# Performance work log

Measured on AMD Instinct MI355X. Metric: run time of the kernel, lower is better.

The kernel has to match this reference:

```python
import jax, jax.numpy as jnp
import numpy as np

N_SRC = 50000
N_DST = 50000
E = 800000
D = 128
OUT = 128


def setup_inputs() -> dict:
    key = jax.random.key(0)
    k1, k2, k3, k4, k5, k6 = jax.random.split(key, 6)
    lim = 1.0 / np.sqrt(D)
    return {
        "x_src": jax.random.normal(k1, (N_SRC, D), dtype=jnp.float32),
        "x_dst": jax.random.normal(k2, (N_DST, D), dtype=jnp.float32),
        "edge_src": jax.random.randint(k3, (E,), 0, N_SRC, dtype=jnp.int64),
        "edge_dst": jax.random.randint(k4, (E,), 0, N_DST, dtype=jnp.int64),
        "num_dst": N_DST,
        # learned params (torch nn.Linear: y = x @ W.T + b), stored here as [in, out]
        "W_neigh": jax.random.uniform(k5, (D, OUT), jnp.float32, -lim, lim),
        "b_neigh": jnp.zeros((OUT,), jnp.float32),
        "W_self": jax.random.uniform(k6, (D, OUT), jnp.float32, -lim, lim),
        "b_self": jnp.zeros((OUT,), jnp.float32),
    }


def reference(x_src, x_dst, edge_src, edge_dst, num_dst, W_neigh, b_neigh, W_self, b_self):
    # gather source features per edge: [E, D]
    neigh_feats = x_src[edge_src]
    # scatter-mean onto destination nodes
    summed = jax.ops.segment_sum(neigh_feats, edge_dst, num_segments=num_dst)  # [num_dst, D]
    count = jax.ops.segment_sum(jnp.ones((edge_dst.shape[0], 1), x_src.dtype), edge_dst,
                                num_segments=num_dst)
    agg = summed / jnp.clip(count, 1.0)
    # dual linear + add
    return agg @ W_neigh + b_neigh + x_dst @ W_self + b_self
```

## Files before the change

### kernel.cpp

```cpp
#include <hip/hip_runtime.h>

#define D 128
#define TM 64
#define RPT 2
#define CBITS 7
#define CSIZE 128
#define MAXNB 512
#define CAPB 2560
#define EPB 2048

typedef __attribute__((ext_vector_type(8))) short bf16x8;
typedef __attribute__((ext_vector_type(4))) float f32x4;


__device__ __forceinline__ unsigned short f32_to_bf16(float x) {
    unsigned u = __float_as_uint(x);
    u += 0x7FFFu + ((u >> 16) & 1u);
    return (unsigned short)(u >> 16);
}
__device__ __forceinline__ float bf16_to_f32(unsigned short h) {
    return __uint_as_float(((unsigned)h) << 16);
}

__global__ __launch_bounds__(256) void prep_kernel(
    const float* __restrict__ Wn, const float* __restrict__ Ws,
    unsigned short* __restrict__ Wtn, unsigned short* __restrict__ Wts,
    int* __restrict__ gcursor, int NB) {
    const int stride = gridDim.x * 256;
    for (int i = blockIdx.x * 256 + threadIdx.x; i < D * D; i += stride) {
        int n = i >> 7, k = i & (D - 1);
        Wtn[i] = f32_to_bf16(Wn[k * D + n]);
        Wts[i] = f32_to_bf16(Ws[k * D + n]);
    }
    for (int i = blockIdx.x * 256 + threadIdx.x; i < NB; i += stride)
        gcursor[i] = 0;
}

__global__ __launch_bounds__(256) void fused_part_gemm_kernel(
    const int* __restrict__ edge_src, const int* __restrict__ edge_dst,
    int* __restrict__ gcursor, int* __restrict__ packed, int E, int NB,
    const float* __restrict__ x_src, const float* __restrict__ x_dst,
    const unsigned short* __restrict__ Wtn, const unsigned short* __restrict__ Wts,
    const float* __restrict__ bn, const float* __restrict__ bs,
    unsigned short* __restrict__ y16, float* __restrict__ out,
    int M_SRC, int N, int nblk, int blkA, int pstride) {
    __shared__ __align__(16) char smem[TM * 136 * 2 + D * 136 * 2];
    const int t = threadIdx.x;
    const int idx = (int)blockIdx.x;

    const bool isPart = (idx % pstride == 0) && (idx / pstride < nblk);

    if (isPart) {
        const int pid = idx / pstride;
        int* lh    = (int*)smem;
        int* lbase = lh + MAXNB;
        for (int i = t; i < NB; i += 256) lh[i] = 0;
        __syncthreads();
        const int base = pid * EPB;
        int es[8], ed[8], rk[8];
        #pragma unroll
        for (int i = 0; i < 8; ++i) {
            int e = base + t + i * 256;
            if (e < E) { es[i] = edge_src[e]; ed[i] = edge_dst[e]; }
            else ed[i] = -1;
        }
        #pragma unroll
        for (int i = 0; i < 8; ++i)
            if (ed[i] >= 0) rk[i] = atomicAdd(&lh[ed[i] >> CBITS], 1);
        __syncthreads();
        for (int i = t; i < NB; i += 256) {
            int v = lh[i];
            lbase[i] = v ? atomicAdd(&gcursor[i], v) : 0;
        }
        __syncthreads();
        #pragma unroll
        for (int i = 0; i < 8; ++i) {
            if (ed[i] >= 0) {
                int bk = ed[i] >> CBITS;
                int pos = lbase[bk] + rk[i];
                if (pos < CAPB)
                    packed[(size_t)bk * CAPB + pos] =
                        (es[i] << CBITS) | (ed[i] & (CSIZE - 1));
            }
        }
        return;
    }

    typedef unsigned short ushort136[136];
    ushort136* LA = (ushort136*)smem;
    ushort136* LW = (ushort136*)(smem + TM * 136 * 2);

    const int npb  = min((idx + pstride - 1) / pstride, nblk);
    const int gb   = idx - npb;
    const bool isA  = gb < blkA;
    const int  base0 = (isA ? gb : gb - blkA) * (TM * RPT);
    const int  M    = isA ? M_SRC : N;
    const float* Ap = isA ? x_src : x_dst;
    const unsigned short* Wp = isA ? Wtn : Wts;

    {
        const int4* Wv = (const int4*)Wp;
        #pragma unroll
        for (int i = 0; i < 8; ++i) {
            int vi = t + i * 256;
            int r = vi >> 4, c8 = vi & 15;
            *(int4*)&LW[r][c8 * 8] = Wv[vi];
        }
    }

    const int lane = t & 63;
    const int wv   = t >> 6;
    const int wr   = wv & 1;
    const int wc   = wv >> 1;
    const int lr   = lane & 15;
    const int g    = lane >> 4;

    #pragma unroll
    for (int half = 0; half < RPT; ++half) {
        const int row0 = base0 + half * TM;
        {
            const float4* Av = (const float4*)Ap;
            #pragma unroll
            for (int i = 0; i < 8; ++i) {
                int vi = t + i * 256;
                int r = vi >> 5, c4 = vi & 31;
                int sr = min(row0 + r, M - 1);
                float4 v = Av[(size_t)sr * 32 + c4];
                ushort4 p;
                p.x = f32_to_bf16(v.x); p.y = f32_to_bf16(v.y);
                p.z = f32_to_bf16(v.z); p.w = f32_to_bf16(v.w);
                *(ushort4*)&LA[r][c4 * 4] = p;
            }
        }
        __syncthreads();

        f32x4 acc[2][4];
        #pragma unroll
        for (int i = 0; i < 2; ++i)
            #pragma unroll
            for (int j = 0; j < 4; ++j) acc[i][j] = (f32x4){0.f, 0.f, 0.f, 0.f};

        #pragma unroll
        for (int kt = 0; kt < 4; ++kt) {
            bf16x8 b0 = *(const bf16x8*)&LW[wc * 64 + 0 * 16 + lr][kt * 32 + g * 8];
            bf16x8 b1 = *(const bf16x8*)&LW[wc * 64 + 1 * 16 + lr][kt * 32 + g * 8];
            bf16x8 b2 = *(const bf16x8*)&LW[wc * 64 + 2 * 16 + lr][kt * 32 + g * 8];
            bf16x8 b3 = *(const bf16x8*)&LW[wc * 64 + 3 * 16 + lr][kt * 32 + g * 8];
            bf16x8 a0 = *(const bf16x8*)&LA[wr * 32 + lr][kt * 32 + g * 8];
            bf16x8 a1 = *(const bf16x8*)&LA[wr * 32 + 16 + lr][kt * 32 + g * 8];
            acc[0][0] = __builtin_amdgcn_mfma_f32_16x16x32_bf16(a0, b0, acc[0][0], 0, 0, 0);
            acc[0][1] = __builtin_amdgcn_mfma_f32_16x16x32_bf16(a0, b1, acc[0][1], 0, 0, 0);
            acc[0][2] = __builtin_amdgcn_mfma_f32_16x16x32_bf16(a0, b2, acc[0][2], 0, 0, 0);
            acc[0][3] = __builtin_amdgcn_mfma_f32_16x16x32_bf16(a0, b3, acc[0][3], 0, 0, 0);
            acc[1][0] = __builtin_amdgcn_mfma_f32_16x16x32_bf16(a1, b0, acc[1][0], 0, 0, 0);
            acc[1][1] = __builtin_amdgcn_mfma_f32_16x16x32_bf16(a1, b1, acc[1][1], 0, 0, 0);
            acc[1][2] = __builtin_amdgcn_mfma_f32_16x16x32_bf16(a1, b2, acc[1][2], 0, 0, 0);
            acc[1][3] = __builtin_amdgcn_mfma_f32_16x16x32_bf16(a1, b3, acc[1][3], 0, 0, 0);
        }

        if (isA) {
            #pragma unroll
            for (int i = 0; i < 2; ++i) {
                #pragma unroll
                for (int j = 0; j < 4; ++j) {
                    int col = wc * 64 + j * 16 + lr;
                    #pragma unroll
                    for (int r = 0; r < 4; ++r) {
                        int row = row0 + wr * 32 + i * 16 + g * 4 + r;
                        if (row < M)
                            y16[(size_t)row * D + col] = f32_to_bf16(acc[i][j][r]);
                    }
                }
            }
        } else {
            #pragma unroll
            for (int i = 0; i < 2; ++i) {
                #pragma unroll
                for (int j = 0; j < 4; ++j) {
                    int col = wc * 64 + j * 16 + lr;
                    float bias = bn[col] + bs[col];
                    #pragma unroll
                    for (int r = 0; r < 4; ++r) {
                        int row = row0 + wr * 32 + i * 16 + g * 4 + r;
                        if (row < M)
                            out[(size_t)row * D + col] = acc[i][j][r] + bias;
                    }
                }
            }
        }
        if (half + 1 < RPT) __syncthreads();
    }
}

__global__ __launch_bounds__(512) void fine_kernel(
    const int* __restrict__ packed, const int* __restrict__ gcursor,
    int* __restrict__ off_beg, int* __restrict__ off_end,
    int* __restrict__ eidx, int N) {
    __shared__ int dcount[8][CSIZE];
    __shared__ int wbase[8][CSIZE];
    __shared__ int sbuf[CSIZE];
    const int b  = blockIdx.x;
    const int d0 = b << CBITS;
    const int beg = b * CAPB;
    const int cnt = min(gcursor[b], CAPB);
    const int t = threadIdx.x;
    const int wv = t >> 6;

    if (t < CSIZE) {
        #pragma unroll
        for (int w = 0; w < 8; ++w) dcount[w][t] = 0;
    }
    __syncthreads();
    for (int i = t; i < cnt; i += 512)
        atomicAdd(&dcount[wv][packed[beg + i] & (CSIZE - 1)], 1);
    __syncthreads();
    int tot = 0;
    if (t < CSIZE) {
        #pragma unroll
        for (int w = 0; w < 8; ++w) tot += dcount[w][t];
        sbuf[t] = tot;
    }
    __syncthreads();
    for (int ofs = 1; ofs < CSIZE; ofs <<= 1) {
        int u = (t < CSIZE && t >= ofs) ? sbuf[t - ofs] : 0;
        __syncthreads();
        if (t < CSIZE) sbuf[t] += u;
        __syncthreads();
    }
    if (t < CSIZE) {
        int excl = sbuf[t] - tot;
        int d = d0 + t;
        if (d < N) {
            off_beg[d] = beg + excl;
            off_end[d] = beg + excl + tot;
        }
        int run = excl;
        #pragma unroll
        for (int w = 0; w < 8; ++w) {
            wbase[w][t] = run;
            run += dcount[w][t];
        }
    }
    __syncthreads();
    for (int i = t; i < cnt; i += 512) {
        int p = packed[beg + i];
        int pos = beg + atomicAdd(&wbase[wv][p & (CSIZE - 1)], 1);
        eidx[pos] = p >> CBITS;
    }
}

__global__ __launch_bounds__(256) void gather_out_kernel(
    const unsigned short* __restrict__ y16,
    const int* __restrict__ off_beg,
    const int* __restrict__ off_end,
    const int* __restrict__ eidx,
    float* __restrict__ out, int N) {
    const int wave = (int)(((long long)blockIdx.x * blockDim.x + threadIdx.x) >> 6);
    const int lane = threadIdx.x & 63;
    if (wave >= N) return;
    const int h = lane >> 4;
    const int c = lane & 15;
    const int beg = off_beg[wave];
    const int end = off_end[wave];

    float acc[8];
    #pragma unroll
    for (int j = 0; j < 8; ++j) acc[j] = 0.f;

    int i = beg + h;
    for (; i + 4 < end; i += 8) {
        int s0 = eidx[i];
        int s1 = eidx[i + 4];
        const int4 v0 = *reinterpret_cast<const int4*>(y16 + (size_t)s0 * D + c * 8);
        const int4 v1 = *reinterpret_cast<const int4*>(y16 + (size_t)s1 * D + c * 8);
        const unsigned short* h0 = (const unsigned short*)&v0;
        const unsigned short* h1 = (const unsigned short*)&v1;
        #pragma unroll
        for (int j = 0; j < 8; ++j)
            acc[j] += bf16_to_f32(h0[j]) + bf16_to_f32(h1[j]);
    }
    if (i < end) {
        int s = eidx[i];
        const int4 v = *reinterpret_cast<const int4*>(y16 + (size_t)s * D + c * 8);
        const unsigned short* hs = (const unsigned short*)&v;
        #pragma unroll
        for (int j = 0; j < 8; ++j) acc[j] += bf16_to_f32(hs[j]);
    }

    #pragma unroll
    for (int j = 0; j < 8; ++j) {
        acc[j] += __shfl_down(acc[j], 32);
        acc[j] += __shfl_down(acc[j], 16);
    }

    if (h == 0) {
        const float inv = 1.0f / fmaxf((float)(end - beg), 1.0f);
        float4* o = reinterpret_cast<float4*>(out + (size_t)wave * D) + c * 2;
        float4 c0 = o[0], c1 = o[1];
        c0.x = fmaf(acc[0], inv, c0.x);
        c0.y = fmaf(acc[1], inv, c0.y);
        c0.z = fmaf(acc[2], inv, c0.z);
        c0.w = fmaf(acc[3], inv, c0.w);
        c1.x = fmaf(acc[4], inv, c1.x);
        c1.y = fmaf(acc[5], inv, c1.y);
        c1.z = fmaf(acc[6], inv, c1.z);
        c1.w = fmaf(acc[7], inv, c1.w);
        o[0] = c0;
        o[1] = c1;
    }
}

extern "C" void kernel_launch(void* const* d_in, const int* in_sizes, int n_in,
                              void* d_out, int out_size, void* d_ws, size_t ws_size,
                              hipStream_t stream) {
    const float* x_src    = (const float*)d_in[0];
    const float* x_dst    = (const float*)d_in[1];
    const int*   edge_src = (const int*)d_in[2];
    const int*   edge_dst = (const int*)d_in[3];
    const float* Wn = (const float*)d_in[5];
    const float* bn = (const float*)d_in[6];
    const float* Ws = (const float*)d_in[7];
    const float* bs = (const float*)d_in[8];

    const int E     = in_sizes[2];
    const int N     = in_sizes[1] / D;
    const int M_SRC = in_sizes[0] / D;

    const int NB   = (N + CSIZE - 1) >> CBITS;
    const int nblk = (E + EPB - 1) / EPB;

    unsigned short* y16 = (unsigned short*)d_ws;
    unsigned short* Wtn = y16 + (size_t)M_SRC * D;
    unsigned short* Wts = Wtn + D * D;
    int* packed  = (int*)(Wts + D * D);
    int* eidx    = packed + (size_t)NB * CAPB;
    int* off_beg = eidx + (size_t)NB * CAPB;
    int* off_end = off_beg + N;
    int* gcursor = off_end + N;

    const int T = 256;
    prep_kernel<<<32, T, 0, stream>>>(Wn, Ws, Wtn, Wts, gcursor, NB);

    const int ROWS = TM * RPT;
    const int blkA = (M_SRC + ROWS - 1) / ROWS;
    const int blkB = (N + ROWS - 1) / ROWS;
    const int total = nblk + blkA + blkB;
    const int pstride = total / nblk > 1 ? total / nblk : 1;
    fused_part_gemm_kernel<<<total, T, 0, stream>>>(
        edge_src, edge_dst, gcursor, packed, E, NB,
        x_src, x_dst, Wtn, Wts, bn, bs, y16, (float*)d_out,
        M_SRC, N, nblk, blkA, pstride);

    fine_kernel<<<NB, 512, 0, stream>>>(packed, gcursor, off_beg, off_end, eidx, N);

    gather_out_kernel<<<(N + 3) / 4, T, 0, stream>>>(
        y16, off_beg, off_end, eidx, (float*)d_out, N);
}
```

Before: 73.77 us.

## Quantize projected source rows to int8 with per-row scales for gather

The projected source features are now stored as int8 with a per-row fp32 scale instead of bf16. Each row's scale comes from a cross-wave absmax reduction staged through shared memory, and rows are written out with coalesced 16-byte stores. The gather kernel reads 16 int8 values per lane plus a scale, which roughly halves the random-gather traffic per edge. The cost is extra syncs and reductions in the GEMM epilogue, plus lower accuracy from int8 quantization that could exceed tolerance.

```diff
diff --git a/kernel.cpp b/kernel.cpp
--- a/kernel.cpp
+++ b/kernel.cpp
@@ -42,7 +42,7 @@
     const float* __restrict__ x_src, const float* __restrict__ x_dst,
     const unsigned short* __restrict__ Wtn, const unsigned short* __restrict__ Wts,
     const float* __restrict__ bn, const float* __restrict__ bs,
-    unsigned short* __restrict__ y16, float* __restrict__ out,
+    char* __restrict__ y8, float* __restrict__ scale_g, float* __restrict__ out,
     int M_SRC, int N, int nblk, int blkA, int pstride) {
     __shared__ __align__(16) char smem[TM * 136 * 2 + D * 136 * 2];
     const int t = threadIdx.x;
@@ -159,18 +159,62 @@
         }
 
         if (isA) {
+            float pmax[2][4];
+            #pragma unroll
+            for (int i = 0; i < 2; ++i)
+                #pragma unroll
+                for (int r = 0; r < 4; ++r) {
+                    float m = fabsf(acc[i][0][r]);
+                    m = fmaxf(m, fabsf(acc[i][1][r]));
+                    m = fmaxf(m, fabsf(acc[i][2][r]));
+                    m = fmaxf(m, fabsf(acc[i][3][r]));
+                    pmax[i][r] = m;
+                }
+            #pragma unroll
+            for (int mask = 1; mask <= 8; mask <<= 1)
+                #pragma unroll
+                for (int i = 0; i < 2; ++i)
+                    #pragma unroll
+                    for (int r = 0; r < 4; ++r)
+                        pmax[i][r] = fmaxf(pmax[i][r], __shfl_xor(pmax[i][r], mask));
+            __syncthreads();
+            float* rmax = (float*)(smem + 8192);
+            char*  st8  = smem;
+            if (lr == 0) {
+                #pragma unroll
+                for (int i = 0; i < 2; ++i)
+                    #pragma unroll
+                    for (int r = 0; r < 4; ++r)
+                        rmax[wc * 64 + wr * 32 + i * 16 + g * 4 + r] = pmax[i][r];
+            }
+            __syncthreads();
             #pragma unroll
             for (int i = 0; i < 2; ++i) {
                 #pragma unroll
-                for (int j = 0; j < 4; ++j) {
-                    int col = wc * 64 + j * 16 + lr;
+                for (int r = 0; r < 4; ++r) {
+                    int rl = wr * 32 + i * 16 + g * 4 + r;
+                    float mx = fmaxf(rmax[rl], rmax[64 + rl]);
+                    float inv = mx > 0.f ? 127.f / mx : 0.f;
                     #pragma unroll
-                    for (int r = 0; r < 4; ++r) {
-                        int row = row0 + wr * 32 + i * 16 + g * 4 + r;
-                        if (row < M)
-                            y16[(size_t)row * D + col] = f32_to_bf16(acc[i][j][r]);
+                    for (int j = 0; j < 4; ++j) {
+                        float v = fmaxf(-127.f, fminf(127.f, acc[i][j][r] * inv));
+                        st8[rl * 128 + wc * 64 + j * 16 + lr] =
+                            (char)__float2int_rn(v);
+                    }
+                    if (lr == 0 && wc == 0) {
+                        int row = row0 + rl;
+                        if (row < M) scale_g[row] = mx * (1.f / 127.f);
                     }
                 }
+            }
+            __syncthreads();
+            #pragma unroll
+            for (int k = 0; k < 2; ++k) {
+                int c16 = t + k * 256;
+                int r = c16 >> 3, off = (c16 & 7) * 16;
+                int row = row0 + r;
+                if (row < M)
+                    *(int4*)(y8 + (size_t)row * D + off) = *(int4*)(st8 + c16 * 16);
             }
         } else {
             #pragma unroll
@@ -250,7 +294,8 @@
 }
 
 __global__ __launch_bounds__(256) void gather_out_kernel(
-    const unsigned short* __restrict__ y16,
+    const char* __restrict__ y8,
+    const float* __restrict__ scale,
     const int* __restrict__ off_beg,
     const int* __restrict__ off_end,
     const int* __restrict__ eidx,
@@ -258,55 +303,57 @@
     const int wave = (int)(((long long)blockIdx.x * blockDim.x + threadIdx.x) >> 6);
     const int lane = threadIdx.x & 63;
     if (wave >= N) return;
-    const int h = lane >> 4;
-    const int c = lane & 15;
+    const int h = lane >> 3;
+    const int c = lane & 7;
     const int beg = off_beg[wave];
     const int end = off_end[wave];
 
-    float acc[8];
+    float acc[16];
     #pragma unroll
-    for (int j = 0; j < 8; ++j) acc[j] = 0.f;
-
-    int i = beg + h;
-    for (; i + 4 < end; i += 8) {
-        int s0 = eidx[i];
-        int s1 = eidx[i + 4];
-        const int4 v0 = *reinterpret_cast<const int4*>(y16 + (size_t)s0 * D + c * 8);
-        const int4 v1 = *reinterpret_cast<const int4*>(y16 + (size_t)s1 * D + c * 8);
-        const unsigned short* h0 = (const unsigned short*)&v0;
-        const unsigned short* h1 = (const unsigned short*)&v1;
-        #pragma unroll
-        for (int j = 0; j < 8; ++j)
-            acc[j] += bf16_to_f32(h0[j]) + bf16_to_f32(h1[j]);
-    }
-    if (i < end) {
+    for (int j = 0; j < 16; ++j) acc[j] = 0.f;
+
+    for (int i = beg + h; i < end; i += 8) {
         int s = eidx[i];
-        const int4 v = *reinterpret_cast<const int4*>(y16 + (size_t)s * D + c * 8);
-        const unsigned short* hs = (const unsigned short*)&v;
-        #pragma unroll
-        for (int j = 0; j < 8; ++j) acc[j] += bf16_to_f32(hs[j]);
+        float sc = scale[s];
+        const int4 v = *reinterpret_cast<const int4*>(y8 + (size_t)s * D + c * 16);
+        const int w0 = v.x, w1 = v.y, w2 = v.z, w3 = v.w;
+        acc[0]  += sc * (float)((w0 << 24) >> 24);
+        acc[1]  += sc * (float)((w0 << 16) >> 24);
+        acc[2]  += sc * (float)((w0 << 8) >> 24);
+        acc[3]  += sc * (float)(w0 >> 24);
+        acc[4]  += sc * (float)((w1 << 24) >> 24);
+        acc[5]  += sc * (float)((w1 << 16) >> 24);
+        acc[6]  += sc * (float)((w1 << 8) >> 24);
+        acc[7]  += sc * (float)(w1 >> 24);
+        acc[8]  += sc * (float)((w2 << 24) >> 24);
+        acc[9]  += sc * (float)((w2 << 16) >> 24);
+        acc[10] += sc * (float)((w2 << 8) >> 24);
+        acc[11] += sc * (float)(w2 >> 24);
+        acc[12] += sc * (float)((w3 << 24) >> 24);
+        acc[13] += sc * (float)((w3 << 16) >> 24);
+        acc[14] += sc * (float)((w3 << 8) >> 24);
+        acc[15] += sc * (float)(w3 >> 24);
     }
 
     #pragma unroll
-    for (int j = 0; j < 8; ++j) {
+    for (int j = 0; j < 16; ++j) {
         acc[j] += __shfl_down(acc[j], 32);
         acc[j] += __shfl_down(acc[j], 16);
+        acc[j] += __shfl_down(acc[j], 8);
     }
 
     if (h == 0) {
         const float inv = 1.0f / fmaxf((float)(end - beg), 1.0f);
-        float4* o = reinterpret_cast<float4*>(out + (size_t)wave * D) + c * 2;
-        float4 c0 = o[0], c1 = o[1];
-        c0.x = fmaf(acc[0], inv, c0.x);
-        c0.y = fmaf(acc[1], inv, c0.y);
-        c0.z = fmaf(acc[2], inv, c0.z);
-        c0.w = fmaf(acc[3], inv, c0.w);
-        c1.x = fmaf(acc[4], inv, c1.x);
-        c1.y = fmaf(acc[5], inv, c1.y);
-        c1.z = fmaf(acc[6], inv, c1.z);
-        c1.w = fmaf(acc[7], inv, c1.w);
-        o[0] = c0;
-        o[1] = c1;
+        float4* o = reinterpret_cast<float4*>(out + (size_t)wave * D + c * 16);
+        #pragma unroll
+        for (int q = 0; q < 4; ++q) {
+            float4 cur = o[q];
+            cur.x = fmaf(acc[q * 4 + 0], inv, cur.x);
+            cur.y = fmaf(acc[q * 4 + 1], inv, cur.y);
+            cur.z = fmaf(acc[q * 4 + 2], inv, cur.z);
+            cur.w = fmaf(acc[q * 4 + 3], inv, cur.w);
+            o[q] = cur;
+        }
     }
 }
 
@@ -329,8 +376,9 @@
     const int NB   = (N + CSIZE - 1) >> CBITS;
     const int nblk = (E + EPB - 1) / EPB;
 
-    unsigned short* y16 = (unsigned short*)d_ws;
-    unsigned short* Wtn = y16 + (size_t)M_SRC * D;
+    char*  y8    = (char*)d_ws;
+    float* scale = (float*)(y8 + (size_t)M_SRC * D);
+    unsigned short* Wtn = (unsigned short*)(scale + M_SRC);
     unsigned short* Wts = Wtn + D * D;
     int* packed  = (int*)(Wts + D * D);
     int* eidx    = packed + (size_t)NB * CAPB;
@@ -348,11 +396,11 @@
     const int pstride = total / nblk > 1 ? total / nblk : 1;
     fused_part_gemm_kernel<<<total, T, 0, stream>>>(
         edge_src, edge_dst, gcursor, packed, E, NB,
-        x_src, x_dst, Wtn, Wts, bn, bs, y16, (float*)d_out,
+        x_src, x_dst, Wtn, Wts, bn, bs, y8, scale, (float*)d_out,
         M_SRC, N, nblk, blkA, pstride);
 
     fine_kernel<<<NB, 512, 0, stream>>>(packed, gcursor, off_beg, off_end, eidx, N);
 
     gather_out_kernel<<<(N + 3) / 4, T, 0, stream>>>(
-        y16, off_beg, off_end, eidx, (float*)d_out, N);
-}
+        y8, scale, off_beg, off_end, eidx, (float*)d_out, N);
+}
```

New measurement: 71.96 us, median of 2. -2.5%, faster.
